# Kernel optimization log

Measured on AMD Instinct MI355X. Metric: run time of the kernel, lower is better.

Reference implementation:

```python
import jax, jax.numpy as jnp
import numpy as np

NH = 16
D = 1024
B, T = 4, 4096


def setup_inputs() -> dict:
    key = jax.random.key(0)
    k1, k2, k3, k4 = jax.random.split(key, 4)
    x = jax.random.normal(k1, (B, T, D), dtype=jnp.float32)
    phi = jax.random.normal(k2, (B, T), dtype=jnp.float32)
    W_attn = jax.random.normal(k3, (D, D), dtype=jnp.float32) * 0.02
    W_proj = jax.random.normal(k4, (D, D), dtype=jnp.float32) * 0.02
    gamma = jnp.ones((NH, 1), dtype=jnp.float32)
    temp = jnp.ones((NH, 1), dtype=jnp.float32)
    return {"x": x, "phi": phi, "W_attn": W_attn, "W_proj": W_proj,
            "gamma": gamma, "temp": temp}


def reference(x, phi, W_attn, W_proj, gamma, temp):
    Bb, Tt, d = x.shape
    hd = d // NH
    # c_attn (no bias), split heads: [B, nh, T, hd]
    w = (x @ W_attn.T).reshape(Bb, Tt, NH, hd).transpose(0, 2, 1, 3)
    w_sq = w * w
    denom = jnp.maximum(jnp.cumsum(w_sq, axis=-2), 1e-12)
    w_norm = w_sq / denom
    tssa_score = w_norm.sum(-1) * temp                       # [B, nh, T]
    phi_Q = phi[:, None, :]                                  # [B, 1, T]
    steps = jnp.arange(1, Tt + 1, dtype=x.dtype)
    mean_phi = jnp.cumsum(phi, axis=-1)[:, None, :] / steps  # running mean of phi
    penalty = (phi_Q - mean_phi) ** 2                        # [B, 1, T]
    score = tssa_score - gamma * penalty                     # [B, nh, T]
    alpha = jax.nn.softmax(score, axis=1)                    # softmax over HEADS (dim=1)
    dots = jnp.cumsum(w_sq * alpha[..., None], axis=-2) / (
        jnp.cumsum(alpha, axis=-1)[..., None] + 1e-8)
    attn = jnp.minimum(1.0 / (1.0 + dots), 10000.0)
    y = -w * alpha[..., None] * attn                          # [B, nh, T, hd]
    y = y.transpose(0, 2, 1, 3).reshape(Bb, Tt, d)
    y = y @ W_proj.T                                          # dropout is identity (p=0 / eval)
    return (y, alpha)
```

## Files before the change

kernel.cpp:

```cpp
#include <hip/hip_runtime.h>
#include <hip/hip_bf16.h>
#include <stdint.h>

#define NHh 16
#define Dm  1024
#define HD  64
#define Bb  4
#define Tt  4096
#define NCH 128
#define CHL 32

#define BM 256
#define BN 256
#define BK 64
#define NKT (Dm / BK)

using bf16 = __hip_bfloat16;
typedef __attribute__((ext_vector_type(8))) short short8;
typedef __attribute__((ext_vector_type(4))) float f32x4;

__device__ __forceinline__ float bf2f(bf16 v) { return __bfloat162float(v); }

__device__ __forceinline__ float b2f(unsigned short u) {
  union { unsigned int i; float f; } x; x.i = ((unsigned int)u) << 16; return x.f;
}

__device__ __forceinline__ float frcp(float x) {
  float r; asm("v_rcp_f32 %0, %1" : "=v"(r) : "v"(x)); return r;
}

__device__ __forceinline__ void gld_lds16(const void* g, void* l) {
  __builtin_amdgcn_global_load_lds(
      (const __attribute__((address_space(1))) unsigned int*)g,
      (__attribute__((address_space(3))) unsigned int*)l, 16, 0, 0);
}

__global__ void cast_f32_to_bf16(const float* __restrict__ in, bf16* __restrict__ out, int n) {
  const int stride = gridDim.x * blockDim.x;
  for (int i = blockIdx.x * blockDim.x + threadIdx.x; i * 4 < n; i += stride) {
    const float4 v = *(const float4*)(in + (size_t)i * 4);
    ushort4 o;
    o.x = __bfloat16_as_ushort(__float2bfloat16(v.x));
    o.y = __bfloat16_as_ushort(__float2bfloat16(v.y));
    o.z = __bfloat16_as_ushort(__float2bfloat16(v.z));
    o.w = __bfloat16_as_ushort(__float2bfloat16(v.w));
    *(ushort4*)(out + (size_t)i * 4) = o;
  }
}

template <bool OUT_BF16, bool WRITE_S1>
__global__ __launch_bounds__(512, 2) void gemm256(const bf16* __restrict__ A,
                                                  const bf16* __restrict__ W,
                                                  void* __restrict__ Cout,
                                                  float* __restrict__ S1,
                                                  int M, int N, int K) {
  extern __shared__ char smem[];
  const int tid  = threadIdx.x;
  const int lane = tid & 63;
  const int wave = tid >> 6;
  const int bid = blockIdx.x;
  const int swz = (bid & 7) * 32 + (bid >> 3);
  const int bn = (swz & 3) * BN;
  const int bm = (swz >> 2) * BM;
  const int wm = (wave >> 2) * 128;
  const int wn = (wave & 3) * 64;
  const int quad = lane >> 4;
  const int l16  = lane & 15;

  const int srow = wave * 8 + (lane >> 3);
  const int scol = (((lane & 7) ^ (lane >> 3)) << 3);

  const bf16* Abase = A + (size_t)(bm + srow) * K + scol;
  const bf16* Wbase = W + (size_t)(bn + srow) * K + scol;

  f32x4 acc[8][4] = {};

#define LDSA(buf, n) (smem + (buf) * 65536 + (n) * 8192 + wave * 1024)
#define LDSB(buf, n) (smem + (buf) * 65536 + 32768 + (n) * 8192 + wave * 1024)

#define STAGE_A(buf, n, k0) gld_lds16(Abase + (size_t)(n) * 64 * K + (k0), LDSA(buf, n))
#define STAGE_B(buf, n, k0) gld_lds16(Wbase + (size_t)(n) * 64 * K + (k0), LDSB(buf, n))

#define LD_FRAG(base, r, s) (*(const short8*)((base) + (size_t)(r) * 128 + ((((s) ^ ((r) & 7))) << 4)))

#pragma unroll
  for (int n = 0; n < 4; n++) STAGE_A(0, n, 0);
#pragma unroll
  for (int n = 0; n < 4; n++) STAGE_B(0, n, 0);
  asm volatile("s_waitcnt vmcnt(0)" ::: "memory");
  __builtin_amdgcn_s_barrier();
  __builtin_amdgcn_sched_barrier(0);

  for (int j = 0; j < NKT; j++) {
    const int buf = j & 1;
    const char* aL = smem + buf * 65536;
    const char* bL = smem + buf * 65536 + 32768;
    const int k0n = (j + 1) * BK;
    const bool pf = (j + 1 < NKT);

    short8 bfv[4][2];
#pragma unroll
    for (int nj = 0; nj < 4; nj++) {
      const int r = wn + nj * 16 + l16;
      bfv[nj][0] = LD_FRAG(bL, r, quad);
      bfv[nj][1] = LD_FRAG(bL, r, quad + 4);
    }
    short8 af[4][2];
#pragma unroll
    for (int mi = 0; mi < 4; mi++) {
      const int r = wm + mi * 16 + l16;
      af[mi][0] = LD_FRAG(aL, r, quad);
      af[mi][1] = LD_FRAG(aL, r, quad + 4);
    }
    if (pf) {
      STAGE_A(buf ^ 1, 0, k0n); STAGE_A(buf ^ 1, 1, k0n);
      STAGE_A(buf ^ 1, 2, k0n); STAGE_A(buf ^ 1, 3, k0n);
    }
    __builtin_amdgcn_s_setprio(1);
#pragma unroll
    for (int mi = 0; mi < 4; mi++)
#pragma unroll
      for (int nj = 0; nj < 4; nj++) {
        acc[mi][nj] = __builtin_amdgcn_mfma_f32_16x16x32_bf16(af[mi][0], bfv[nj][0], acc[mi][nj], 0, 0, 0);
        acc[mi][nj] = __builtin_amdgcn_mfma_f32_16x16x32_bf16(af[mi][1], bfv[nj][1], acc[mi][nj], 0, 0, 0);
      }
    __builtin_amdgcn_s_setprio(0);
    __builtin_amdgcn_sched_barrier(0);

#pragma unroll
    for (int mi = 0; mi < 4; mi++) {
      const int r = wm + 64 + mi * 16 + l16;
      af[mi][0] = LD_FRAG(aL, r, quad);
      af[mi][1] = LD_FRAG(aL, r, quad + 4);
    }
    if (pf) {
      STAGE_B(buf ^ 1, 0, k0n); STAGE_B(buf ^ 1, 1, k0n);
      STAGE_B(buf ^ 1, 2, k0n); STAGE_B(buf ^ 1, 3, k0n);
    }
    __builtin_amdgcn_s_setprio(1);
#pragma unroll
    for (int mi = 0; mi < 4; mi++)
#pragma unroll
      for (int nj = 0; nj < 4; nj++) {
        acc[mi + 4][nj] = __builtin_amdgcn_mfma_f32_16x16x32_bf16(af[mi][0], bfv[nj][0], acc[mi + 4][nj], 0, 0, 0);
        acc[mi + 4][nj] = __builtin_amdgcn_mfma_f32_16x16x32_bf16(af[mi][1], bfv[nj][1], acc[mi + 4][nj], 0, 0, 0);
      }
    __builtin_amdgcn_s_setprio(0);

    asm volatile("s_waitcnt vmcnt(0)" ::: "memory");
    __builtin_amdgcn_s_barrier();
    __builtin_amdgcn_sched_barrier(0);
  }

#pragma unroll
  for (int nj = 0; nj < 4; nj++) {
    const int col = bn + wn + nj * 16 + l16;
    if constexpr (OUT_BF16) {
      float ss0 = 0.f, ss1 = 0.f, ss2 = 0.f, ss3 = 0.f;
#pragma unroll
      for (int mi = 0; mi < 8; mi++) {
        float csum = 0.f;
#pragma unroll
        for (int r = 0; r < 4; r++) {
          const int row = bm + wm + mi * 16 + quad * 4 + r;
          const bf16 hv = __float2bfloat16(acc[mi][nj][r]);
          ((bf16*)Cout)[(size_t)row * N + col] = hv;
          if constexpr (WRITE_S1) { const float fv = bf2f(hv); csum += fv * fv; }
        }
        if constexpr (WRITE_S1) {
          if (mi < 2) ss0 += csum;
          else if (mi < 4) ss1 += csum;
          else if (mi < 6) ss2 += csum;
          else ss3 += csum;
        }
      }
      if constexpr (WRITE_S1) {
        ss0 += __shfl_xor(ss0, 16, 64); ss0 += __shfl_xor(ss0, 32, 64);
        ss1 += __shfl_xor(ss1, 16, 64); ss1 += __shfl_xor(ss1, 32, 64);
        ss2 += __shfl_xor(ss2, 16, 64); ss2 += __shfl_xor(ss2, 32, 64);
        ss3 += __shfl_xor(ss3, 16, 64); ss3 += __shfl_xor(ss3, 32, 64);
        if (quad == 0) {
          const int h = col >> 6, d = col & 63;
          const int r0 = bm + wm;
          const int b  = r0 >> 12;
          const int c0 = (r0 & (Tt - 1)) >> 5;
          float* s1p = S1 + (((size_t)(b * NHh + h) * NCH) + c0) * HD + d;
          s1p[0]      = ss0;
          s1p[HD]     = ss1;
          s1p[2 * HD] = ss2;
          s1p[3 * HD] = ss3;
        }
      }
    } else {
#pragma unroll
      for (int mi = 0; mi < 8; mi++)
#pragma unroll
        for (int r = 0; r < 4; r++) {
          const int row = bm + wm + mi * 16 + quad * 4 + r;
          ((float*)Cout)[(size_t)row * N + col] = acc[mi][nj][r];
        }
    }
  }
#undef LDSA
#undef LDSB
#undef STAGE_A
#undef STAGE_B
#undef LD_FRAG
}

__global__ __launch_bounds__(1024) void phi_penalty_kernel(const float* __restrict__ phi,
                                                           float* __restrict__ penalty) {
  const int b = blockIdx.x;
  const int tid = threadIdx.x;
  const int lane = tid & 63, wid = tid >> 6;
  __shared__ float wsum[16];
  __shared__ float carry_s;
  if (tid == 0) carry_s = 0.f;
  __syncthreads();
  for (int r = 0; r < Tt / 1024; r++) {
    const int t = r * 1024 + tid;
    const float v = phi[b * Tt + t];
    float incl = v;
#pragma unroll
    for (int off = 1; off < 64; off <<= 1) {
      float n = __shfl_up(incl, off, 64);
      if (lane >= off) incl += n;
    }
    if (lane == 63) wsum[wid] = incl;
    __syncthreads();
    float woff = carry_s;
    for (int wpre = 0; wpre < wid; wpre++) woff += wsum[wpre];
    const float csum = woff + incl;
    const float mean = csum / (float)(t + 1);
    const float dphi = v - mean;
    penalty[b * Tt + t] = dphi * dphi;
    __syncthreads();
    if (tid == 0) {
      float s = 0.f;
      for (int w = 0; w < 16; w++) s += wsum[w];
      carry_s += s;
    }
    __syncthreads();
  }
}

__global__ __launch_bounds__(64) void prefix_vec(float* __restrict__ S) {
  __shared__ float tile[NCH * HD];
  const int bh = blockIdx.x, tid = threadIdx.x;
  float* p = S + (size_t)bh * NCH * HD;
  const float4* src = (const float4*)p;
  float4* dst = (float4*)tile;
#pragma unroll 4
  for (int k = 0; k < (NCH * HD / 4) / 64; k++) dst[k * 64 + tid] = src[k * 64 + tid];
  __syncthreads();
  float run = 0.f;
  for (int c = 0; c < NCH; c++) {
    const float v = tile[c * HD + tid];
    tile[c * HD + tid] = run;
    run += v;
  }
  __syncthreads();
  float4* out = (float4*)p;
#pragma unroll 4
  for (int k = 0; k < (NCH * HD / 4) / 64; k++) out[k * 64 + tid] = dst[k * 64 + tid];
}

__global__ __launch_bounds__(64) void prefix_dots(float* __restrict__ S2, float* __restrict__ SA) {
  __shared__ float tile[NCH * HD];
  const int bh = blockIdx.x, tid = threadIdx.x;
  float* q = SA + (size_t)bh * NCH;
  const float v0 = q[tid], v1 = q[64 + tid];
  float i0 = v0;
#pragma unroll
  for (int off = 1; off < 64; off <<= 1) {
    const float n = __shfl_up(i0, off, 64);
    if (tid >= off) i0 += n;
  }
  const float tot0 = __shfl(i0, 63, 64);
  float i1 = v1;
#pragma unroll
  for (int off = 1; off < 64; off <<= 1) {
    const float n = __shfl_up(i1, off, 64);
    if (tid >= off) i1 += n;
  }
  i1 += tot0;
  q[tid] = i0 - v0;
  q[64 + tid] = i1 - v1;
  float* p = S2 + (size_t)bh * NCH * HD;
  const float4* src = (const float4*)p;
  float4* dst = (float4*)tile;
#pragma unroll 4
  for (int k = 0; k < (NCH * HD / 4) / 64; k++) dst[k * 64 + tid] = src[k * 64 + tid];
  __syncthreads();
  float run = 0.f;
  for (int c = 0; c < NCH; c++) {
    const float v = tile[c * HD + tid];
    tile[c * HD + tid] = run;
    run += v;
  }
  __syncthreads();
  float4* out = (float4*)p;
#pragma unroll 4
  for (int k = 0; k < (NCH * HD / 4) / 64; k++) out[k * 64 + tid] = dst[k * 64 + tid];
}

__global__ __launch_bounds__(64) void tssa_phase3(const bf16* __restrict__ w,
                                                  const float* __restrict__ Sex,
                                                  const float* __restrict__ temp,
                                                  float* __restrict__ tssa) {
  const int g = threadIdx.x >> 4, l = threadIdx.x & 15;
  const int c = blockIdx.x * 4 + g, h = blockIdx.y, b = blockIdx.z;
  const float4 ex = *(const float4*)&Sex[(((size_t)(b * NHh + h) * NCH) + c) * HD + l * 4];
  float a0 = ex.x, a1 = ex.y, a2 = ex.z, a3 = ex.w;
  const bf16* wp = w + ((size_t)(b * Tt + c * CHL)) * Dm + h * HD + l * 4;
  const float tv = temp[h];
  float* op = tssa + ((size_t)(b * Tt + c * CHL)) * NHh + h;
#pragma unroll 8
  for (int i = 0; i < CHL; i++) {
    const ushort4 v = *(const ushort4*)(wp + (size_t)i * Dm);
    const float f0 = b2f(v.x), f1 = b2f(v.y), f2 = b2f(v.z), f3 = b2f(v.w);
    const float s0 = f0 * f0, s1 = f1 * f1, s2 = f2 * f2, s3 = f3 * f3;
    a0 += s0; a1 += s1; a2 += s2; a3 += s3;
    float val = s0 * frcp(fmaxf(a0, 1e-12f)) + s1 * frcp(fmaxf(a1, 1e-12f))
              + s2 * frcp(fmaxf(a2, 1e-12f)) + s3 * frcp(fmaxf(a3, 1e-12f));
    val += __shfl_xor(val, 1, 64);
    val += __shfl_xor(val, 2, 64);
    val += __shfl_xor(val, 4, 64);
    val += __shfl_xor(val, 8, 64);
    if (l == 0) op[(size_t)i * NHh] = tv * val;
  }
}

__global__ void softmax_heads(const float* __restrict__ tssa, const float* __restrict__ penalty,
                              const float* __restrict__ gamma, float* __restrict__ alpha_f) {
  const int idx = blockIdx.x * blockDim.x + threadIdx.x;
  const int b = idx >> 12;
  const int t = idx & 4095;
  const float pen = penalty[idx];
  float sc[NHh];
  const float4* tp = (const float4*)(tssa + (size_t)idx * NHh);
#pragma unroll
  for (int q = 0; q < 4; q++) {
    const float4 v = tp[q];
    sc[q * 4 + 0] = v.x; sc[q * 4 + 1] = v.y; sc[q * 4 + 2] = v.z; sc[q * 4 + 3] = v.w;
  }
  float mx = -1e30f;
#pragma unroll
  for (int h = 0; h < NHh; h++) {
    sc[h] -= gamma[h] * pen;
    mx = fmaxf(mx, sc[h]);
  }
  float sum = 0.f;
#pragma unroll
  for (int h = 0; h < NHh; h++) { const float e = __expf(sc[h] - mx); sc[h] = e; sum += e; }
  const float inv = 1.f / sum;
#pragma unroll
  for (int h = 0; h < NHh; h++) {
    alpha_f[((size_t)(b * NHh + h)) * Tt + t] = sc[h] * inv;
  }
}

__global__ __launch_bounds__(64) void dots_phase1(const bf16* __restrict__ w,
                                                  const float* __restrict__ alpha_f,
                                                  float* __restrict__ S2, float* __restrict__ SA) {
  const int g = threadIdx.x >> 4, l = threadIdx.x & 15;
  const int c = blockIdx.x * 4 + g, h = blockIdx.y, b = blockIdx.z;
  const bf16* wp = w + ((size_t)(b * Tt + c * CHL)) * Dm + h * HD + l * 4;
  const float* ap = alpha_f + (size_t)(b * NHh + h) * Tt + c * CHL;
  float a0 = 0.f, a1 = 0.f, a2 = 0.f, a3 = 0.f, acca = 0.f;
#pragma unroll 8
  for (int i = 0; i < CHL; i++) {
    const float a = ap[i];
    const ushort4 v = *(const ushort4*)(wp + (size_t)i * Dm);
    const float f0 = b2f(v.x), f1 = b2f(v.y), f2 = b2f(v.z), f3 = b2f(v.w);
    a0 += f0 * f0 * a; a1 += f1 * f1 * a; a2 += f2 * f2 * a; a3 += f3 * f3 * a;
    acca += a;
  }
  float4 o; o.x = a0; o.y = a1; o.z = a2; o.w = a3;
  *(float4*)&S2[(((size_t)(b * NHh + h) * NCH) + c) * HD + l * 4] = o;
  if (l == 0) SA[(size_t)(b * NHh + h) * NCH + c] = acca;
}

__global__ __launch_bounds__(64) void y_phase3(const bf16* __restrict__ w,
                                               const float* __restrict__ alpha_f,
                                               const float* __restrict__ S2ex,
                                               const float* __restrict__ SAex,
                                               bf16* __restrict__ yprime) {
  const int g = threadIdx.x >> 4, l = threadIdx.x & 15;
  const int c = blockIdx.x * 4 + g, h = blockIdx.y, b = blockIdx.z;
  const float4 ex = *(const float4*)&S2ex[(((size_t)(b * NHh + h) * NCH) + c) * HD + l * 4];
  float a0 = ex.x, a1 = ex.y, a2 = ex.z, a3 = ex.w;
  float acca = SAex[(size_t)(b * NHh + h) * NCH + c];
  const bf16* wp = w + ((size_t)(b * Tt + c * CHL)) * Dm + h * HD + l * 4;
  const float* ap = alpha_f + (size_t)(b * NHh + h) * Tt + c * CHL;
  bf16* yp = yprime + ((size_t)(b * Tt + c * CHL)) * Dm + h * HD + l * 4;
#pragma unroll 8
  for (int i = 0; i < CHL; i++) {
    const float a = ap[i];
    const ushort4 v = *(const ushort4*)(wp + (size_t)i * Dm);
    const float f0 = b2f(v.x), f1 = b2f(v.y), f2 = b2f(v.z), f3 = b2f(v.w);
    a0 += f0 * f0 * a; a1 += f1 * f1 * a; a2 += f2 * f2 * a; a3 += f3 * f3 * a;
    acca += a;
    const float rinv = frcp(acca + 1e-8f);
    const float at0 = fminf(frcp(1.f + a0 * rinv), 10000.f);
    const float at1 = fminf(frcp(1.f + a1 * rinv), 10000.f);
    const float at2 = fminf(frcp(1.f + a2 * rinv), 10000.f);
    const float at3 = fminf(frcp(1.f + a3 * rinv), 10000.f);
    ushort4 o;
    o.x = __bfloat16_as_ushort(__float2bfloat16(-f0 * a * at0));
    o.y = __bfloat16_as_ushort(__float2bfloat16(-f1 * a * at1));
    o.z = __bfloat16_as_ushort(__float2bfloat16(-f2 * a * at2));
    o.w = __bfloat16_as_ushort(__float2bfloat16(-f3 * a * at3));
    *(ushort4*)(yp + (size_t)i * Dm) = o;
  }
}

extern "C" void kernel_launch(void* const* d_in, const int* in_sizes, int n_in,
                              void* d_out, int out_size, void* d_ws, size_t ws_size,
                              hipStream_t stream) {
  const float* x     = (const float*)d_in[0];
  const float* phi   = (const float*)d_in[1];
  const float* Wattn = (const float*)d_in[2];
  const float* Wproj = (const float*)d_in[3];
  const float* gamma = (const float*)d_in[4];
  const float* temp  = (const float*)d_in[5];

  float* y_out    = (float*)d_out;
  float* alpha_f  = y_out + (size_t)Bb * Tt * Dm;

  char* ws = (char*)d_ws;
  bf16*  x_bf   = (bf16*)ws;  ws += (size_t)Bb * Tt * Dm * 2;
  bf16*  Wa_bf  = (bf16*)ws;  ws += (size_t)Dm * Dm * 2;
  bf16*  Wp_bf  = (bf16*)ws;  ws += (size_t)Dm * Dm * 2;
  bf16*  w_bf   = (bf16*)ws;  ws += (size_t)Bb * Tt * Dm * 2;
  float* tssa   = (float*)ws; ws += (size_t)Bb * Tt * NHh * 4;
  float* pen    = (float*)ws; ws += (size_t)Bb * Tt * 4;
  float* S1     = (float*)ws; ws += (size_t)Bb * NHh * NCH * HD * 4;
  float* S2     = (float*)ws; ws += (size_t)Bb * NHh * NCH * HD * 4;
  float* SA     = (float*)ws; ws += (size_t)Bb * NHh * NCH * 4;
  bf16*  yprime = x_bf;

  static int attr_done = 0;
  if (!attr_done) {
    hipFuncSetAttribute((const void*)gemm256<true, true>,
                        hipFuncAttributeMaxDynamicSharedMemorySize, 131072);
    hipFuncSetAttribute((const void*)gemm256<false, false>,
                        hipFuncAttributeMaxDynamicSharedMemorySize, 131072);
    attr_done = 1;
  }

  const int M = Bb * Tt, N = Dm, K = Dm;
  dim3 gg((M / BM) * (N / BN)), gb(512);
  dim3 g3(NCH / 4, NHh, Bb), b64(64);

  cast_f32_to_bf16<<<dim3(1024), dim3(256), 0, stream>>>(x, x_bf, Bb * Tt * Dm);
  cast_f32_to_bf16<<<dim3(256), dim3(256), 0, stream>>>(Wattn, Wa_bf, Dm * Dm);
  cast_f32_to_bf16<<<dim3(256), dim3(256), 0, stream>>>(Wproj, Wp_bf, Dm * Dm);

  gemm256<true, true><<<gg, gb, 131072, stream>>>(x_bf, Wa_bf, (void*)w_bf, S1, M, N, K);
  phi_penalty_kernel<<<dim3(Bb), dim3(1024), 0, stream>>>(phi, pen);
  prefix_vec<<<dim3(Bb * NHh), b64, 0, stream>>>(S1);
  tssa_phase3<<<g3, b64, 0, stream>>>(w_bf, S1, temp, tssa);
  softmax_heads<<<dim3(Bb * Tt / 256), dim3(256), 0, stream>>>(tssa, pen, gamma, alpha_f);
  dots_phase1<<<g3, b64, 0, stream>>>(w_bf, alpha_f, S2, SA);
  prefix_dots<<<dim3(Bb * NHh), b64, 0, stream>>>(S2, SA);
  y_phase3<<<g3, b64, 0, stream>>>(w_bf, alpha_f, S2, SA, yprime);
  gemm256<false, false><<<gg, gb, 131072, stream>>>(yprime, Wp_bf, (void*)y_out, nullptr, M, N, K);
}
```

Before: 264.0 us.

## Fuse tssa, head softmax and dots phase; rework GEMM wave tiling and pipelining

Three middle kernels (tssa score, softmax over heads, dots chunk sums) become one kernel per (chunk, batch). It keeps the scores and alpha in shared memory, so the tssa buffer and a reread of alpha go away, as do two launches. The GEMM wave layout changes from 2x4 (128x64) to 4x2 (64x128) per wave. Prefetch of the next tile is split across both half-iterations, with partial vmcnt waits instead of a full drain. The risks are wrong vmcnt counts and a different register and LDS-read balance in the GEMM.

```diff
diff --git a/kernel.cpp b/kernel.cpp
--- a/kernel.cpp
+++ b/kernel.cpp
@@ -62,8 +62,8 @@
   const int swz = (bid & 7) * 32 + (bid >> 3);
   const int bn = (swz & 3) * BN;
   const int bm = (swz >> 2) * BM;
-  const int wm = (wave >> 2) * 128;
-  const int wn = (wave & 3) * 64;
+  const int wm = (wave >> 1) * 64;
+  const int wn = (wave & 1) * 128;
   const int quad = lane >> 4;
   const int l16  = lane & 15;
 
@@ -73,48 +73,44 @@
   const bf16* Abase = A + (size_t)(bm + srow) * K + scol;
   const bf16* Wbase = W + (size_t)(bn + srow) * K + scol;
 
-  f32x4 acc[8][4] = {};
-
-#define LDSA(buf, n) (smem + (buf) * 65536 + (n) * 8192 + wave * 1024)
-#define LDSB(buf, n) (smem + (buf) * 65536 + 32768 + (n) * 8192 + wave * 1024)
-
-#define STAGE_A(buf, n, k0) gld_lds16(Abase + (size_t)(n) * 64 * K + (k0), LDSA(buf, n))
-#define STAGE_B(buf, n, k0) gld_lds16(Wbase + (size_t)(n) * 64 * K + (k0), LDSB(buf, n))
-
+  f32x4 acc[4][8] = {};
+
+#define SLAB_A(buf, n) (smem + (buf) * 65536 + (n) * 8192 + wave * 1024)
+#define SLAB_B(buf, n) (smem + (buf) * 65536 + 32768 + (n) * 8192 + wave * 1024)
+#define STAGE_A(buf, n, k0) gld_lds16(Abase + (size_t)(n) * 64 * K + (k0), SLAB_A(buf, n))
+#define STAGE_B(buf, n, k0) gld_lds16(Wbase + (size_t)(n) * 64 * K + (k0), SLAB_B(buf, n))
 #define LD_FRAG(base, r, s) (*(const short8*)((base) + (size_t)(r) * 128 + ((((s) ^ ((r) & 7))) << 4)))
 
-#pragma unroll
-  for (int n = 0; n < 4; n++) STAGE_A(0, n, 0);
-#pragma unroll
-  for (int n = 0; n < 4; n++) STAGE_B(0, n, 0);
+  STAGE_A(0, 0, 0); STAGE_A(0, 1, 0); STAGE_A(0, 2, 0); STAGE_A(0, 3, 0);
+  STAGE_B(0, 0, 0); STAGE_B(0, 1, 0); STAGE_B(0, 2, 0); STAGE_B(0, 3, 0);
   asm volatile("s_waitcnt vmcnt(0)" ::: "memory");
   __builtin_amdgcn_s_barrier();
   __builtin_amdgcn_sched_barrier(0);
 
-  for (int j = 0; j < NKT; j++) {
-    const int buf = j & 1;
+  short8 af[4][2], bfv[4][2];
+  for (int t = 0; t < NKT; t++) {
+    const int buf = t & 1;
     const char* aL = smem + buf * 65536;
-    const char* bL = smem + buf * 65536 + 32768;
-    const int k0n = (j + 1) * BK;
-    const bool pf = (j + 1 < NKT);
-
-    short8 bfv[4][2];
+    const char* bL = aL + 32768;
+    const int k0n = (t + 1) * BK;
+    const bool pf = (t + 1 < NKT);
+
+    if (pf) {
+      STAGE_A(buf ^ 1, 0, k0n); STAGE_A(buf ^ 1, 1, k0n);
+      STAGE_A(buf ^ 1, 2, k0n); STAGE_A(buf ^ 1, 3, k0n);
+      STAGE_B(buf ^ 1, 0, k0n); STAGE_B(buf ^ 1, 2, k0n);
+    }
+#pragma unroll
+    for (int mi = 0; mi < 4; mi++) {
+      const int r = wm + mi * 16 + l16;
+      af[mi][0] = LD_FRAG(aL, r, quad);
+      af[mi][1] = LD_FRAG(aL, r, quad + 4);
+    }
 #pragma unroll
     for (int nj = 0; nj < 4; nj++) {
       const int r = wn + nj * 16 + l16;
       bfv[nj][0] = LD_FRAG(bL, r, quad);
       bfv[nj][1] = LD_FRAG(bL, r, quad + 4);
-    }
-    short8 af[4][2];
-#pragma unroll
-    for (int mi = 0; mi < 4; mi++) {
-      const int r = wm + mi * 16 + l16;
-      af[mi][0] = LD_FRAG(aL, r, quad);
-      af[mi][1] = LD_FRAG(aL, r, quad + 4);
-    }
-    if (pf) {
-      STAGE_A(buf ^ 1, 0, k0n); STAGE_A(buf ^ 1, 1, k0n);
-      STAGE_A(buf ^ 1, 2, k0n); STAGE_A(buf ^ 1, 3, k0n);
     }
     __builtin_amdgcn_s_setprio(1);
 #pragma unroll
@@ -125,40 +121,39 @@
         acc[mi][nj] = __builtin_amdgcn_mfma_f32_16x16x32_bf16(af[mi][1], bfv[nj][1], acc[mi][nj], 0, 0, 0);
       }
     __builtin_amdgcn_s_setprio(0);
+    if (pf) { asm volatile("s_waitcnt vmcnt(6)" ::: "memory"); }
+    else    { asm volatile("s_waitcnt vmcnt(0)" ::: "memory"); }
+    __builtin_amdgcn_s_barrier();
     __builtin_amdgcn_sched_barrier(0);
 
-#pragma unroll
-    for (int mi = 0; mi < 4; mi++) {
-      const int r = wm + 64 + mi * 16 + l16;
-      af[mi][0] = LD_FRAG(aL, r, quad);
-      af[mi][1] = LD_FRAG(aL, r, quad + 4);
-    }
-    if (pf) {
-      STAGE_B(buf ^ 1, 0, k0n); STAGE_B(buf ^ 1, 1, k0n);
-      STAGE_B(buf ^ 1, 2, k0n); STAGE_B(buf ^ 1, 3, k0n);
+    if (pf) { STAGE_B(buf ^ 1, 1, k0n); STAGE_B(buf ^ 1, 3, k0n); }
+#pragma unroll
+    for (int nj = 0; nj < 4; nj++) {
+      const int r = wn + 64 + nj * 16 + l16;
+      bfv[nj][0] = LD_FRAG(bL, r, quad);
+      bfv[nj][1] = LD_FRAG(bL, r, quad + 4);
     }
     __builtin_amdgcn_s_setprio(1);
 #pragma unroll
     for (int mi = 0; mi < 4; mi++)
 #pragma unroll
       for (int nj = 0; nj < 4; nj++) {
-        acc[mi + 4][nj] = __builtin_amdgcn_mfma_f32_16x16x32_bf16(af[mi][0], bfv[nj][0], acc[mi + 4][nj], 0, 0, 0);
-        acc[mi + 4][nj] = __builtin_amdgcn_mfma_f32_16x16x32_bf16(af[mi][1], bfv[nj][1], acc[mi + 4][nj], 0, 0, 0);
+        acc[mi][nj + 4] = __builtin_amdgcn_mfma_f32_16x16x32_bf16(af[mi][0], bfv[nj][0], acc[mi][nj + 4], 0, 0, 0);
+        acc[mi][nj + 4] = __builtin_amdgcn_mfma_f32_16x16x32_bf16(af[mi][1], bfv[nj][1], acc[mi][nj + 4], 0, 0, 0);
       }
     __builtin_amdgcn_s_setprio(0);
-
-    asm volatile("s_waitcnt vmcnt(0)" ::: "memory");
+    asm volatile("s_waitcnt vmcnt(2)" ::: "memory");
     __builtin_amdgcn_s_barrier();
     __builtin_amdgcn_sched_barrier(0);
   }
 
 #pragma unroll
-  for (int nj = 0; nj < 4; nj++) {
+  for (int nj = 0; nj < 8; nj++) {
     const int col = bn + wn + nj * 16 + l16;
     if constexpr (OUT_BF16) {
-      float ss0 = 0.f, ss1 = 0.f, ss2 = 0.f, ss3 = 0.f;
-#pragma unroll
-      for (int mi = 0; mi < 8; mi++) {
+      float ss0 = 0.f, ss1 = 0.f;
+#pragma unroll
+      for (int mi = 0; mi < 4; mi++) {
         float csum = 0.f;
 #pragma unroll
         for (int r = 0; r < 4; r++) {
@@ -167,33 +162,24 @@
           ((bf16*)Cout)[(size_t)row * N + col] = hv;
           if constexpr (WRITE_S1) { const float fv = bf2f(hv); csum += fv * fv; }
         }
-        if constexpr (WRITE_S1) {
-          if (mi < 2) ss0 += csum;
-          else if (mi < 4) ss1 += csum;
-          else if (mi < 6) ss2 += csum;
-          else ss3 += csum;
-        }
+        if constexpr (WRITE_S1) { if (mi < 2) ss0 += csum; else ss1 += csum; }
       }
       if constexpr (WRITE_S1) {
         ss0 += __shfl_xor(ss0, 16, 64); ss0 += __shfl_xor(ss0, 32, 64);
         ss1 += __shfl_xor(ss1, 16, 64); ss1 += __shfl_xor(ss1, 32, 64);
-        ss2 += __shfl_xor(ss2, 16, 64); ss2 += __shfl_xor(ss2, 32, 64);
-        ss3 += __shfl_xor(ss3, 16, 64); ss3 += __shfl_xor(ss3, 32, 64);
         if (quad == 0) {
           const int h = col >> 6, d = col & 63;
           const int r0 = bm + wm;
           const int b  = r0 >> 12;
           const int c0 = (r0 & (Tt - 1)) >> 5;
           float* s1p = S1 + (((size_t)(b * NHh + h) * NCH) + c0) * HD + d;
-          s1p[0]      = ss0;
-          s1p[HD]     = ss1;
-          s1p[2 * HD] = ss2;
-          s1p[3 * HD] = ss3;
+          s1p[0]  = ss0;
+          s1p[HD] = ss1;
         }
       }
     } else {
 #pragma unroll
-      for (int mi = 0; mi < 8; mi++)
+      for (int mi = 0; mi < 4; mi++)
 #pragma unroll
         for (int r = 0; r < 4; r++) {
           const int row = bm + wm + mi * 16 + quad * 4 + r;
@@ -201,8 +187,8 @@
         }
     }
   }
-#undef LDSA
-#undef LDSB
+#undef SLAB_A
+#undef SLAB_B
 #undef STAGE_A
 #undef STAGE_B
 #undef LD_FRAG
@@ -304,17 +290,26 @@
   for (int k = 0; k < (NCH * HD / 4) / 64; k++) out[k * 64 + tid] = dst[k * 64 + tid];
 }
 
-__global__ __launch_bounds__(64) void tssa_phase3(const bf16* __restrict__ w,
-                                                  const float* __restrict__ Sex,
-                                                  const float* __restrict__ temp,
-                                                  float* __restrict__ tssa) {
-  const int g = threadIdx.x >> 4, l = threadIdx.x & 15;
-  const int c = blockIdx.x * 4 + g, h = blockIdx.y, b = blockIdx.z;
-  const float4 ex = *(const float4*)&Sex[(((size_t)(b * NHh + h) * NCH) + c) * HD + l * 4];
+__global__ __launch_bounds__(256) void mid_fused(const bf16* __restrict__ w,
+                                                 const float* __restrict__ S1ex,
+                                                 const float* __restrict__ temp,
+                                                 const float* __restrict__ gamma,
+                                                 const float* __restrict__ penalty,
+                                                 float* __restrict__ alpha_f,
+                                                 float* __restrict__ S2,
+                                                 float* __restrict__ SA) {
+  const int c = blockIdx.x, b = blockIdx.y;
+  const int tid = threadIdx.x, h = tid >> 4, l = tid & 15;
+  __shared__ float sm_t[CHL][NHh + 1];
+  __shared__ float sm_a[CHL][NHh + 1];
+  __shared__ float sm_g[NHh], sm_tv[NHh];
+  if (tid < NHh) { sm_g[tid] = gamma[tid]; sm_tv[tid] = temp[tid]; }
+  __syncthreads();
+
+  const bf16* wp = w + ((size_t)(b * Tt + c * CHL)) * Dm + h * HD + l * 4;
+  const float4 ex = *(const float4*)&S1ex[(((size_t)(b * NHh + h) * NCH) + c) * HD + l * 4];
   float a0 = ex.x, a1 = ex.y, a2 = ex.z, a3 = ex.w;
-  const bf16* wp = w + ((size_t)(b * Tt + c * CHL)) * Dm + h * HD + l * 4;
-  const float tv = temp[h];
-  float* op = tssa + ((size_t)(b * Tt + c * CHL)) * NHh + h;
+  const float tv = sm_tv[h];
 #pragma unroll 8
   for (int i = 0; i < CHL; i++) {
     const ushort4 v = *(const ushort4*)(wp + (size_t)i * Dm);
@@ -327,58 +322,47 @@
     val += __shfl_xor(val, 2, 64);
     val += __shfl_xor(val, 4, 64);
     val += __shfl_xor(val, 8, 64);
-    if (l == 0) op[(size_t)i * NHh] = tv * val;
-  }
-}
-
-__global__ void softmax_heads(const float* __restrict__ tssa, const float* __restrict__ penalty,
-                              const float* __restrict__ gamma, float* __restrict__ alpha_f) {
-  const int idx = blockIdx.x * blockDim.x + threadIdx.x;
-  const int b = idx >> 12;
-  const int t = idx & 4095;
-  const float pen = penalty[idx];
-  float sc[NHh];
-  const float4* tp = (const float4*)(tssa + (size_t)idx * NHh);
-#pragma unroll
-  for (int q = 0; q < 4; q++) {
-    const float4 v = tp[q];
-    sc[q * 4 + 0] = v.x; sc[q * 4 + 1] = v.y; sc[q * 4 + 2] = v.z; sc[q * 4 + 3] = v.w;
-  }
-  float mx = -1e30f;
-#pragma unroll
-  for (int h = 0; h < NHh; h++) {
-    sc[h] -= gamma[h] * pen;
-    mx = fmaxf(mx, sc[h]);
-  }
-  float sum = 0.f;
-#pragma unroll
-  for (int h = 0; h < NHh; h++) { const float e = __expf(sc[h] - mx); sc[h] = e; sum += e; }
-  const float inv = 1.f / sum;
-#pragma unroll
-  for (int h = 0; h < NHh; h++) {
-    alpha_f[((size_t)(b * NHh + h)) * Tt + t] = sc[h] * inv;
-  }
-}
-
-__global__ __launch_bounds__(64) void dots_phase1(const bf16* __restrict__ w,
-                                                  const float* __restrict__ alpha_f,
-                                                  float* __restrict__ S2, float* __restrict__ SA) {
-  const int g = threadIdx.x >> 4, l = threadIdx.x & 15;
-  const int c = blockIdx.x * 4 + g, h = blockIdx.y, b = blockIdx.z;
-  const bf16* wp = w + ((size_t)(b * Tt + c * CHL)) * Dm + h * HD + l * 4;
-  const float* ap = alpha_f + (size_t)(b * NHh + h) * Tt + c * CHL;
-  float a0 = 0.f, a1 = 0.f, a2 = 0.f, a3 = 0.f, acca = 0.f;
+    if (l == 0) sm_t[i][h] = tv * val;
+  }
+  __syncthreads();
+
+  if (tid < CHL) {
+    const int t = tid;
+    const float pen = penalty[(size_t)b * Tt + c * CHL + t];
+    float sc[NHh];
+    float mx = -1e30f;
+#pragma unroll
+    for (int hh = 0; hh < NHh; hh++) {
+      sc[hh] = sm_t[t][hh] - sm_g[hh] * pen;
+      mx = fmaxf(mx, sc[hh]);
+    }
+    float sum = 0.f;
+#pragma unroll
+    for (int hh = 0; hh < NHh; hh++) { const float e = __expf(sc[hh] - mx); sc[hh] = e; sum += e; }
+    const float inv = 1.f / sum;
+#pragma unroll
+    for (int hh = 0; hh < NHh; hh++) sm_a[t][hh] = sc[hh] * inv;
+  }
+  __syncthreads();
+
+#pragma unroll
+  for (int k2 = 0; k2 < CHL / 16; k2++) {
+    const int t = k2 * 16 + l;
+    alpha_f[((size_t)(b * NHh + h)) * Tt + c * CHL + t] = sm_a[t][h];
+  }
+
+  float d0 = 0.f, d1 = 0.f, d2 = 0.f, d3 = 0.f, sa = 0.f;
 #pragma unroll 8
   for (int i = 0; i < CHL; i++) {
-    const float a = ap[i];
+    const float a = sm_a[i][h];
     const ushort4 v = *(const ushort4*)(wp + (size_t)i * Dm);
     const float f0 = b2f(v.x), f1 = b2f(v.y), f2 = b2f(v.z), f3 = b2f(v.w);
-    a0 += f0 * f0 * a; a1 += f1 * f1 * a; a2 += f2 * f2 * a; a3 += f3 * f3 * a;
-    acca += a;
-  }
-  float4 o; o.x = a0; o.y = a1; o.z = a2; o.w = a3;
+    d0 += f0 * f0 * a; d1 += f1 * f1 * a; d2 += f2 * f2 * a; d3 += f3 * f3 * a;
+    sa += a;
+  }
+  float4 o; o.x = d0; o.y = d1; o.z = d2; o.w = d3;
   *(float4*)&S2[(((size_t)(b * NHh + h) * NCH) + c) * HD + l * 4] = o;
-  if (l == 0) SA[(size_t)(b * NHh + h) * NCH + c] = acca;
+  if (l == 0) SA[(size_t)(b * NHh + h) * NCH + c] = sa;
 }
 
 __global__ __launch_bounds__(64) void y_phase3(const bf16* __restrict__ w,
@@ -433,7 +417,6 @@
   bf16*  Wa_bf  = (bf16*)ws;  ws += (size_t)Dm * Dm * 2;
   bf16*  Wp_bf  = (bf16*)ws;  ws += (size_t)Dm * Dm * 2;
   bf16*  w_bf   = (bf16*)ws;  ws += (size_t)Bb * Tt * Dm * 2;
-  float* tssa   = (float*)ws; ws += (size_t)Bb * Tt * NHh * 4;
   float* pen    = (float*)ws; ws += (size_t)Bb * Tt * 4;
   float* S1     = (float*)ws; ws += (size_t)Bb * NHh * NCH * HD * 4;
   float* S2     = (float*)ws; ws += (size_t)Bb * NHh * NCH * HD * 4;
@@ -460,9 +443,8 @@
   gemm256<true, true><<<gg, gb, 131072, stream>>>(x_bf, Wa_bf, (void*)w_bf, S1, M, N, K);
   phi_penalty_kernel<<<dim3(Bb), dim3(1024), 0, stream>>>(phi, pen);
   prefix_vec<<<dim3(Bb * NHh), b64, 0, stream>>>(S1);
-  tssa_phase3<<<g3, b64, 0, stream>>>(w_bf, S1, temp, tssa);
-  softmax_heads<<<dim3(Bb * Tt / 256), dim3(256), 0, stream>>>(tssa, pen, gamma, alpha_f);
-  dots_phase1<<<g3, b64, 0, stream>>>(w_bf, alpha_f, S2, SA);
+  mid_fused<<<dim3(NCH, Bb), dim3(256), 0, stream>>>(w_bf, S1, temp, gamma, pen,
+                                                     alpha_f, S2, SA);
   prefix_dots<<<dim3(Bb * NHh), b64, 0, stream>>>(S2, SA);
   y_phase3<<<g3, b64, 0, stream>>>(w_bf, alpha_f, S2, SA, yprime);
   gemm256<false, false><<<gg, gb, 131072, stream>>>(yprime, Wp_bf, (void*)y_out, nullptr, M, N, K);
```

After: 260.8 us. No clear change (-1.2%).
